# Kernel optimization log

Measured on AMD Instinct MI355X. Metric: run time of the kernel, lower is better.

The kernel has to match this reference:

```python
import jax, jax.numpy as jnp
import numpy as np

TAU = 0.1
LAMBD = 0.75
EPS = 1e-8  # torch cosine_similarity norm clamp


def setup_inputs() -> dict:
    key = jax.random.key(0)
    k1, k2 = jax.random.split(key)
    B, D = 8192, 768
    v = jax.random.normal(k1, (B, D), dtype=jnp.float32)
    u = jax.random.normal(k2, (B, D), dtype=jnp.float32)
    return {"v": v, "u": u}


def reference(v, u):
    # Batched equivalent of the per-sample Python loop:
    # cos(v_i, u_j) = <v_i/||v_i||, u_j/||u_j||>, with torch's eps clamp on norms.
    v = v.astype(jnp.float32)
    u = u.astype(jnp.float32)
    vn = v / jnp.maximum(jnp.linalg.norm(v, axis=1, keepdims=True), EPS)
    un = u / jnp.maximum(jnp.linalg.norm(u, axis=1, keepdims=True), EPS)
    sim = jnp.einsum('id,jd->ij', vn, un) / TAU  # [B, B] logits
    diag = jnp.diagonal(sim)
    # image->text: -log( exp(sim_ii) / sum_j exp(sim_ij) )
    loss_it = jax.nn.logsumexp(sim, axis=1) - diag
    # text->image: -log( exp(sim_ii) / sum_j exp(sim_ji) )
    loss_ti = jax.nn.logsumexp(sim, axis=0) - diag
    # In the torch source text_image calls .item(), detaching it from autograd.
    loss_ti = jax.lax.stop_gradient(loss_ti)
    return jnp.mean(LAMBD * loss_it + (1.0 - LAMBD) * loss_ti)
```

## Files before the change

kernel.cpp:

```cpp
#include <hip/hip_runtime.h>
#include <hip/hip_bf16.h>

typedef unsigned char u8;
typedef unsigned short u16;
typedef unsigned int u32;
typedef float f32x16 __attribute__((ext_vector_type(16)));
typedef int i32x4 __attribute__((ext_vector_type(4)));
typedef int i32x8 __attribute__((ext_vector_type(8)));

#define B_SZ 8192
#define D_SZ 768
#define TAU_INV 10.0f
#define ESCALE 0.014088818758681283f
#define FP4_SCALE 32.0f
#define SCHRAU_K1 118185.58f
#define SCHRAU_K2 1064879685.0f


__device__ __forceinline__ u32 fp4_enc(float x) {
    float y = fabsf(x);
    u32 n = (u32)(y >= 0.25f) + (u32)(y >= 0.75f) + (u32)(y >= 1.25f) +
            (u32)(y >= 1.75f) + (u32)(y >= 2.5f)  + (u32)(y >= 3.5f) +
            (u32)(y >= 5.0f);
    return n | (x < 0.f ? 8u : 0u);
}

__device__ __forceinline__ u16 fp4_pack4(float x, float y, float z, float w) {
    return (u16)(fp4_enc(x) | (fp4_enc(y) << 4) | (fp4_enc(z) << 8) | (fp4_enc(w) << 12));
}

__global__ __launch_bounds__(256) void norm_kernel(const float4* __restrict__ v,
                                                   const float4* __restrict__ u,
                                                   u16* __restrict__ vn,
                                                   u16* __restrict__ un,
                                                   float* __restrict__ diag) {
    const int wid = threadIdx.x >> 6, lane = threadIdx.x & 63;
    const int row = blockIdx.x * 4 + wid;
    const float4* vr = v + (size_t)row * 192;
    const float4* ur = u + (size_t)row * 192;
    float4 a[3], b[3];
    float sv = 0.f, su = 0.f, sd = 0.f;
#pragma unroll
    for (int c = 0; c < 3; ++c) {
        a[c] = vr[lane + 64 * c];
        b[c] = ur[lane + 64 * c];
        sv += a[c].x * a[c].x + a[c].y * a[c].y + a[c].z * a[c].z + a[c].w * a[c].w;
        su += b[c].x * b[c].x + b[c].y * b[c].y + b[c].z * b[c].z + b[c].w * b[c].w;
        sd += a[c].x * b[c].x + a[c].y * b[c].y + a[c].z * b[c].z + a[c].w * b[c].w;
    }
#pragma unroll
    for (int m = 1; m < 64; m <<= 1) {
        sv += __shfl_xor(sv, m);
        su += __shfl_xor(su, m);
        sd += __shfl_xor(sd, m);
    }
    const float iv = FP4_SCALE / fmaxf(sqrtf(sv), 1e-8f);
    const float iu = FP4_SCALE / fmaxf(sqrtf(su), 1e-8f);
    const int rg = row >> 5, rr = row & 31;
#pragma unroll
    for (int c = 0; c < 3; ++c) {
        u16 pa = fp4_pack4(a[c].x * iv, a[c].y * iv, a[c].z * iv, a[c].w * iv);
        u16 pb = fp4_pack4(b[c].x * iu, b[c].y * iu, b[c].z * iu, b[c].w * iu);
        const int e = lane + 64 * c;
        const int idx = (rg * 12 + (e >> 4)) * 512 + ((e >> 3) & 1) * 256 + rr * 8 + (e & 7);
        vn[idx] = pa;
        un[idx] = pb;
    }
    if (lane == 0) diag[row] = sd * iv * iu * TAU_INV / (FP4_SCALE * FP4_SCALE);
}

__device__ __forceinline__ i32x8 ldfrag4(const u8* __restrict__ base, u32 off) {
    i32x4 lo = *(const i32x4*)(base + off);
    return __builtin_shufflevector(lo, lo, 0, 1, 2, 3, 0, 1, 2, 3);
}

__device__ __forceinline__ f32x16 mx_mfma4(i32x8 a, i32x8 b, f32x16 c) {
    return __builtin_amdgcn_mfma_scale_f32_32x32x64_f8f6f4(
        a, b, c, 4, 4, 0, 0x7F7F7F7F, 0, 0x7F7F7F7F);
}

__global__ __launch_bounds__(256, 4) void simexp_kernel(const u8* __restrict__ vn,
                                                        const u8* __restrict__ un,
                                                        float* __restrict__ rowP,
                                                        float* __restrict__ colP) {
    __shared__ float rowLds[2][128];
    __shared__ float colLds[2][128];

    const int tid  = threadIdx.x;
    const int wid  = tid >> 6;
    const int lane = tid & 63;
    const int l32  = lane & 31;
    const int h    = lane >> 5;
    const int wr = wid >> 1, wc = wid & 1;

    const int id = blockIdx.x;
    const int chunk = id >> 6;
    const int li = id & 63;
    const int rb = ((chunk >> 3) << 3) + (li >> 3);
    const int cb = ((chunk & 7) << 3) + (li & 7);

    const int aBase = __builtin_amdgcn_readfirstlane((rb * 4 + wr * 2) * 12288);
    const int bBase = __builtin_amdgcn_readfirstlane((cb * 4 + wc * 2) * 12288);
    const u8* __restrict__ A0 = vn + aBase;
    const u8* __restrict__ A1 = A0 + 12288;
    const u8* __restrict__ B0 = un + bBase;
    const u8* __restrict__ B1 = B0 + 12288;
    u32 voff = (u32)lane * 16;

    f32x16 acc[2][2];
#pragma unroll
    for (int i = 0; i < 2; ++i)
#pragma unroll
        for (int j = 0; j < 2; ++j)
#pragma unroll
            for (int r = 0; r < 16; ++r) acc[i][j][r] = 0.f;

    i32x8 fa[2][2], fb[2][2];

#define LOAD_SLOT(s)                        \
    {                                       \
        fa[s][0] = ldfrag4(A0, voff);       \
        fa[s][1] = ldfrag4(A1, voff);       \
        fb[s][0] = ldfrag4(B0, voff);       \
        fb[s][1] = ldfrag4(B1, voff);       \
        voff += 1024;                       \
    }
#define MFMA_SLOT(s)                                          \
    {                                                         \
        acc[0][0] = mx_mfma4(fa[s][0], fb[s][0], acc[0][0]);  \
        acc[1][0] = mx_mfma4(fa[s][1], fb[s][0], acc[1][0]);  \
        acc[0][1] = mx_mfma4(fa[s][0], fb[s][1], acc[0][1]);  \
        acc[1][1] = mx_mfma4(fa[s][1], fb[s][1], acc[1][1]);  \
    }

    LOAD_SLOT(0)
#pragma unroll 1
    for (int it = 0; it < 12; it += 2) {
        LOAD_SLOT(1)
        MFMA_SLOT(0)
        if (it + 2 < 12) LOAD_SLOT(0)
        MFMA_SLOT(1)
    }

    float rowAcc[32];
    float colAcc[2];
#pragma unroll
    for (int t = 0; t < 32; ++t) rowAcc[t] = 0.f;
    colAcc[0] = 0.f; colAcc[1] = 0.f;
#pragma unroll
    for (int i = 0; i < 2; ++i)
#pragma unroll
        for (int j = 0; j < 2; ++j)
#pragma unroll
            for (int r = 0; r < 16; ++r) {
                float t = fmaf(acc[i][j][r], SCHRAU_K1, SCHRAU_K2);
                float e = __int_as_float((int)t);
                rowAcc[i * 16 + r] += e;
                colAcc[j] += e;
            }
#pragma unroll
    for (int m = 1; m < 32; m <<= 1)
#pragma unroll
        for (int t = 0; t < 32; ++t) rowAcc[t] += __shfl_xor(rowAcc[t], m);
    colAcc[0] += __shfl_xor(colAcc[0], 32);
    colAcc[1] += __shfl_xor(colAcc[1], 32);

#pragma unroll
    for (int i = 0; i < 2; ++i)
#pragma unroll
        for (int t = 0; t < 16; ++t)
            if (l32 == t) {
                int row = wr * 64 + i * 32 + (t & 3) + 8 * (t >> 2) + 4 * h;
                rowLds[wc][row] = rowAcc[i * 16 + t];
            }
    if (h == 0) {
#pragma unroll
        for (int j = 0; j < 2; ++j)
            colLds[wr][wc * 64 + j * 32 + l32] = colAcc[j];
    }
    __syncthreads();
    if (tid < 128) {
        rowP[(size_t)cb * B_SZ + rb * 128 + tid] = rowLds[0][tid] + rowLds[1][tid];
    } else {
        const int t = tid - 128;
        colP[(size_t)rb * B_SZ + cb * 128 + t] = colLds[0][t] + colLds[1][t];
    }
}

__global__ __launch_bounds__(256) void finalize_kernel(const float* __restrict__ rowP,
                                                       const float* __restrict__ colP,
                                                       const float* __restrict__ diag,
                                                       float* __restrict__ out) {
    const int i = blockIdx.x * 256 + threadIdx.x;
    float rs = 0.f, cs = 0.f;
#pragma unroll 8
    for (int p = 0; p < 64; ++p) {
        rs += rowP[(size_t)p * B_SZ + i];
        cs += colP[(size_t)p * B_SZ + i];
    }
    float contrib = (0.75f * logf(rs) + 0.25f * logf(cs) - diag[i]) * (1.0f / (float)B_SZ);
#pragma unroll
    for (int m = 1; m < 64; m <<= 1) contrib += __shfl_xor(contrib, m);
    __shared__ float red[4];
    const int wid = threadIdx.x >> 6, lane = threadIdx.x & 63;
    if (lane == 0) red[wid] = contrib;
    __syncthreads();
    if (threadIdx.x == 0) atomicAdd(out, red[0] + red[1] + red[2] + red[3]);
}

extern "C" void kernel_launch(void* const* d_in, const int* in_sizes, int n_in,
                              void* d_out, int out_size, void* d_ws, size_t ws_size,
                              hipStream_t stream) {
    const float* v = (const float*)d_in[0];
    const float* u = (const float*)d_in[1];
    char* ws = (char*)d_ws;
    u16* vn4   = (u16*)(ws);
    u16* un4   = (u16*)(ws + 3145728);
    float* dg  = (float*)(ws + 6291456);
    float* rwp = (float*)(ws + 6324224);
    float* clp = (float*)(ws + 8421376);
    float* out = (float*)d_out;

    hipMemsetAsync(out, 0, sizeof(float), stream);
    hipLaunchKernelGGL(norm_kernel, dim3(2048), dim3(256), 0, stream,
                       (const float4*)v, (const float4*)u, vn4, un4, dg);
    hipLaunchKernelGGL(simexp_kernel, dim3(4096), dim3(256), 0, stream,
                       (const u8*)vn4, (const u8*)un4, rwp, clp);
    hipLaunchKernelGGL(finalize_kernel, dim3(B_SZ / 256), dim3(256), 0, stream, rwp, clp, dg, out);
}
```

Measured before the change: 140.2 us.

## Enlarge similarity tile to 256x128 per block with 4x2 MFMA accumulators

```diff
diff --git a/kernel.cpp b/kernel.cpp
--- a/kernel.cpp
+++ b/kernel.cpp
@@ -79,11 +79,11 @@
         a, b, c, 4, 4, 0, 0x7F7F7F7F, 0, 0x7F7F7F7F);
 }
 
-__global__ __launch_bounds__(256, 4) void simexp_kernel(const u8* __restrict__ vn,
+__global__ __launch_bounds__(256, 2) void simexp_kernel(const u8* __restrict__ vn,
                                                         const u8* __restrict__ un,
                                                         float* __restrict__ rowP,
                                                         float* __restrict__ colP) {
-    __shared__ float rowLds[2][128];
+    __shared__ float rowLds[2][256];
     __shared__ float colLds[2][128];
 
     const int tid  = threadIdx.x;
@@ -99,38 +99,46 @@
     const int rb = ((chunk >> 3) << 3) + (li >> 3);
     const int cb = ((chunk & 7) << 3) + (li & 7);
 
-    const int aBase = __builtin_amdgcn_readfirstlane((rb * 4 + wr * 2) * 12288);
-    const int bBase = __builtin_amdgcn_readfirstlane((cb * 4 + wc * 2) * 12288);
-    const u8* __restrict__ A0 = vn + aBase;
+    const int aB = __builtin_amdgcn_readfirstlane((rb * 8 + wr * 4) * 12288);
+    const int bB = __builtin_amdgcn_readfirstlane((cb * 4 + wc * 2) * 12288);
+    const u8* __restrict__ A0 = vn + aB;
     const u8* __restrict__ A1 = A0 + 12288;
-    const u8* __restrict__ B0 = un + bBase;
+    const u8* __restrict__ A2 = A0 + 2 * 12288;
+    const u8* __restrict__ A3 = A0 + 3 * 12288;
+    const u8* __restrict__ B0 = un + bB;
     const u8* __restrict__ B1 = B0 + 12288;
     u32 voff = (u32)lane * 16;
 
-    f32x16 acc[2][2];
-#pragma unroll
-    for (int i = 0; i < 2; ++i)
+    f32x16 acc[4][2];
+#pragma unroll
+    for (int i = 0; i < 4; ++i)
 #pragma unroll
         for (int j = 0; j < 2; ++j)
 #pragma unroll
             for (int r = 0; r < 16; ++r) acc[i][j][r] = 0.f;
 
-    i32x8 fa[2][2], fb[2][2];
+    i32x8 fa[2][4], fb[2][2];
 
 #define LOAD_SLOT(s)                        \
     {                                       \
         fa[s][0] = ldfrag4(A0, voff);       \
         fa[s][1] = ldfrag4(A1, voff);       \
+        fa[s][2] = ldfrag4(A2, voff);       \
+        fa[s][3] = ldfrag4(A3, voff);       \
         fb[s][0] = ldfrag4(B0, voff);       \
         fb[s][1] = ldfrag4(B1, voff);       \
         voff += 1024;                       \
     }
-#define MFMA_SLOT(s)                                          \
-    {                                                         \
-        acc[0][0] = mx_mfma4(fa[s][0], fb[s][0], acc[0][0]);  \
-        acc[1][0] = mx_mfma4(fa[s][1], fb[s][0], acc[1][0]);  \
-        acc[0][1] = mx_mfma4(fa[s][0], fb[s][1], acc[0][1]);  \
-        acc[1][1] = mx_mfma4(fa[s][1], fb[s][1], acc[1][1]);  \
+#define MFMA_SLOT(s)                                           \
+    {                                                          \
+        acc[0][0] = mx_mfma4(fa[s][0], fb[s][0], acc[0][0]);   \
+        acc[1][0] = mx_mfma4(fa[s][1], fb[s][0], acc[1][0]);   \
+        acc[2][0] = mx_mfma4(fa[s][2], fb[s][0], acc[2][0]);   \
+        acc[3][0] = mx_mfma4(fa[s][3], fb[s][0], acc[3][0]);   \
+        acc[0][1] = mx_mfma4(fa[s][0], fb[s][1], acc[0][1]);   \
+        acc[1][1] = mx_mfma4(fa[s][1], fb[s][1], acc[1][1]);   \
+        acc[2][1] = mx_mfma4(fa[s][2], fb[s][1], acc[2][1]);   \
+        acc[3][1] = mx_mfma4(fa[s][3], fb[s][1], acc[3][1]);   \
     }
 
     LOAD_SLOT(0)
@@ -142,13 +150,13 @@
         MFMA_SLOT(1)
     }
 
-    float rowAcc[32];
+    float rowAcc[64];
     float colAcc[2];
 #pragma unroll
-    for (int t = 0; t < 32; ++t) rowAcc[t] = 0.f;
+    for (int t = 0; t < 64; ++t) rowAcc[t] = 0.f;
     colAcc[0] = 0.f; colAcc[1] = 0.f;
 #pragma unroll
-    for (int i = 0; i < 2; ++i)
+    for (int i = 0; i < 4; ++i)
 #pragma unroll
         for (int j = 0; j < 2; ++j)
 #pragma unroll
@@ -161,16 +169,16 @@
 #pragma unroll
     for (int m = 1; m < 32; m <<= 1)
 #pragma unroll
-        for (int t = 0; t < 32; ++t) rowAcc[t] += __shfl_xor(rowAcc[t], m);
+        for (int t = 0; t < 64; ++t) rowAcc[t] += __shfl_xor(rowAcc[t], m);
     colAcc[0] += __shfl_xor(colAcc[0], 32);
     colAcc[1] += __shfl_xor(colAcc[1], 32);
 
 #pragma unroll
-    for (int i = 0; i < 2; ++i)
+    for (int i = 0; i < 4; ++i)
 #pragma unroll
         for (int t = 0; t < 16; ++t)
             if (l32 == t) {
-                int row = wr * 64 + i * 32 + (t & 3) + 8 * (t >> 2) + 4 * h;
+                int row = wr * 128 + i * 32 + (t & 3) + 8 * (t >> 2) + 4 * h;
                 rowLds[wc][row] = rowAcc[i * 16 + t];
             }
     if (h == 0) {
@@ -179,12 +187,9 @@
             colLds[wr][wc * 64 + j * 32 + l32] = colAcc[j];
     }
     __syncthreads();
-    if (tid < 128) {
-        rowP[(size_t)cb * B_SZ + rb * 128 + tid] = rowLds[0][tid] + rowLds[1][tid];
-    } else {
-        const int t = tid - 128;
-        colP[(size_t)rb * B_SZ + cb * 128 + t] = colLds[0][t] + colLds[1][t];
-    }
+    rowP[(size_t)cb * B_SZ + rb * 256 + tid] = rowLds[0][tid] + rowLds[1][tid];
+    if (tid < 128)
+        colP[(size_t)rb * B_SZ + cb * 128 + tid] = colLds[0][tid] + colLds[1][tid];
 }
 
 __global__ __launch_bounds__(256) void finalize_kernel(const float* __restrict__ rowP,
@@ -194,10 +199,9 @@
     const int i = blockIdx.x * 256 + threadIdx.x;
     float rs = 0.f, cs = 0.f;
 #pragma unroll 8
-    for (int p = 0; p < 64; ++p) {
-        rs += rowP[(size_t)p * B_SZ + i];
-        cs += colP[(size_t)p * B_SZ + i];
-    }
+    for (int p = 0; p < 64; ++p) rs += rowP[(size_t)p * B_SZ + i];
+#pragma unroll 8
+    for (int p = 0; p < 32; ++p) cs += colP[(size_t)p * B_SZ + i];
     float contrib = (0.75f * logf(rs) + 0.25f * logf(cs) - diag[i]) * (1.0f / (float)B_SZ);
 #pragma unroll
     for (int m = 1; m < 64; m <<= 1) contrib += __shfl_xor(contrib, m);
@@ -224,7 +228,7 @@
     hipMemsetAsync(out, 0, sizeof(float), stream);
     hipLaunchKernelGGL(norm_kernel, dim3(2048), dim3(256), 0, stream,
                        (const float4*)v, (const float4*)u, vn4, un4, dg);
-    hipLaunchKernelGGL(simexp_kernel, dim3(4096), dim3(256), 0, stream,
+    hipLaunchKernelGGL(simexp_kernel, dim3(2048), dim3(256), 0, stream,
                        (const u8*)vn4, (const u8*)un4, rwp, clp);
     hipLaunchKernelGGL(finalize_kernel, dim3(B_SZ / 256), dim3(256), 0, stream, rwp, clp, dg, out);
 }
```

Result: slower. 144.6 us (+3.1%).
